# Optimization experiments

Measured on AMD Instinct MI355X. Metric: run time of the kernel, lower is better.

The kernel has to match this reference:

```python
import jax, jax.numpy as jnp
import numpy as np

B, S, D, H, DH = 2, 2048, 2048, 16, 128
ROT_DIM = 128
ROT_BASE = 10000.0
ATTN_SCALE = float(np.sqrt(DH))


def _sin_cos_rotary(n_ctx, rotary_dim, base):
    pos = jnp.arange(n_ctx, dtype=jnp.float32)
    dim = jnp.arange(rotary_dim // 2, dtype=jnp.float32)
    freq = base ** (dim / (rotary_dim / 2))
    freq = jnp.concatenate([freq, freq])  # non-adjacent pairs: '(2 d)' layout
    angles = pos[:, None] / freq[None, :]  # [n_ctx, rotary_dim]
    return jnp.sin(angles), jnp.cos(angles)


def _rotate_every_two(x):
    # non-adjacent-pairs rotation: [-x2, x1] on halves of last dim
    d = x.shape[-1]
    return jnp.concatenate([-x[..., d // 2:], x[..., :d // 2]], axis=-1)


def _apply_rotary(x, sin, cos):
    # x: [batch, pos, head, d_head]
    n = x.shape[1]
    x_rot = x[..., :ROT_DIM]
    x_pass = x[..., ROT_DIM:]
    c = cos[:n][None, :, None, :]
    s = sin[:n][None, :, None, :]
    x_rotated = x_rot * c + _rotate_every_two(x_rot) * s
    return jnp.concatenate([x_rotated, x_pass], axis=-1)


def setup_inputs() -> dict:
    key = jax.random.key(0)
    ks = jax.random.split(key, 8)
    init = 0.02
    return {
        'query_input': jax.random.normal(ks[0], (B, S, D), jnp.float32),
        'key_input': jax.random.normal(ks[1], (B, S, D), jnp.float32),
        'value_input': jax.random.normal(ks[2], (B, S, D), jnp.float32),
        'W_Q': jax.random.normal(ks[3], (H, D, DH), jnp.float32) * init,
        'W_K': jax.random.normal(ks[4], (H, D, DH), jnp.float32) * init,
        'W_V': jax.random.normal(ks[5], (H, D, DH), jnp.float32) * init,
        'W_O': jax.random.normal(ks[6], (H, DH, D), jnp.float32) * init,
        'b_Q': jnp.zeros((H, DH), jnp.float32),
        'b_K': jnp.zeros((H, DH), jnp.float32),
        'b_V': jnp.zeros((H, DH), jnp.float32),
        'b_O': jnp.zeros((D,), jnp.float32),
    }


def reference(query_input, key_input, value_input, W_Q, W_K, W_V, W_O, b_Q, b_K, b_V, b_O):
    # QKV projections: [b, pos, d_model] x [h, d_model, d_head] -> [b, pos, h, d_head]
    q = jnp.einsum('bpd,hde->bphe', query_input, W_Q) + b_Q
    k = jnp.einsum('bpd,hde->bphe', key_input, W_K) + b_K
    v = jnp.einsum('bpd,hde->bphe', value_input, W_V) + b_V

    sin, cos = _sin_cos_rotary(S, ROT_DIM, ROT_BASE)
    q = _apply_rotary(q, sin, cos)
    k = _apply_rotary(k, sin, cos)

    # attention scores [b, h, q_pos, k_pos]
    scores = jnp.einsum('bqhe,bkhe->bhqk', q, k) / ATTN_SCALE
    causal = jnp.tril(jnp.ones((S, S), bool))
    scores = jnp.where(causal[None, None], scores, -jnp.inf)
    pattern = jax.nn.softmax(scores, axis=-1)
    pattern = jnp.where(jnp.isnan(pattern), jnp.zeros_like(pattern), pattern)

    z = jnp.einsum('bhqk,bkhe->bqhe', pattern, v)
    out = jnp.einsum('bqhe,hed->bqd', z, W_O) + b_O
    return out
```

## Files before the change

### kernel.cpp

```cpp
#include <hip/hip_runtime.h>
#include <hip/hip_bf16.h>
#include <cmath>

typedef __bf16 bf16;
typedef __bf16 bf16x8 __attribute__((ext_vector_type(8)));
typedef __bf16 bf16x4 __attribute__((ext_vector_type(4)));
typedef float  f32x4  __attribute__((ext_vector_type(4)));


__global__ void xcvt_kernel(const float* __restrict__ a, const float* __restrict__ b,
                            const float* __restrict__ c,
                            bf16* __restrict__ oa, bf16* __restrict__ ob, bf16* __restrict__ oc) {
    int i = (blockIdx.x * 256 + threadIdx.x) * 4;
    float4 va = *(const float4*)(a + i);
    float4 vb = *(const float4*)(b + i);
    float4 vc = *(const float4*)(c + i);
    bf16x4 ra = { (bf16)va.x, (bf16)va.y, (bf16)va.z, (bf16)va.w };
    bf16x4 rb = { (bf16)vb.x, (bf16)vb.y, (bf16)vb.z, (bf16)vb.w };
    bf16x4 rc = { (bf16)vc.x, (bf16)vc.y, (bf16)vc.z, (bf16)vc.w };
    *(bf16x4*)(oa + i) = ra;
    *(bf16x4*)(ob + i) = rb;
    *(bf16x4*)(oc + i) = rc;
}

__global__ void wtr_kernel(const float* __restrict__ WQ, const float* __restrict__ WK,
                           const float* __restrict__ WV, const float* __restrict__ WO,
                           bf16* __restrict__ WQT, bf16* __restrict__ WKT,
                           bf16* __restrict__ WVT, bf16* __restrict__ WOT) {
    __shared__ float T[64 * 65];
    const int z = blockIdx.y;
    const int bx = blockIdx.x;
    const int tid = threadIdx.x;
    const int tr = tid >> 4;
    const int tc = (tid & 15) * 4;

    const float* src; bf16* dst;
    long sbase, dbase; int sRS;
    if (z < 3) {
        src = (z == 0) ? WQ : (z == 1) ? WK : WV;
        dst = (z == 0) ? WQT : (z == 1) ? WKT : WVT;
        int h = bx >> 6, rem = bx & 63;
        int d0 = (rem >> 1) << 6, e0 = (rem & 1) << 6;
        sbase = (long)h * 262144 + (long)d0 * 128 + e0;
        sRS = 128;
        dbase = (long)(h * 128 + e0) * 2048 + d0;
    } else {
        src = WO; dst = WOT;
        int a0 = (bx >> 5) << 6, b0 = (bx & 31) << 6;
        sbase = (long)a0 * 2048 + b0;
        sRS = 2048;
        dbase = (long)b0 * 2048 + a0;
    }

#pragma unroll
    for (int p = 0; p < 4; p++) {
        int r = p * 16 + tr;
        float4 v = *(const float4*)(src + sbase + (long)r * sRS + tc);
        T[r * 65 + tc]     = v.x;
        T[r * 65 + tc + 1] = v.y;
        T[r * 65 + tc + 2] = v.z;
        T[r * 65 + tc + 3] = v.w;
    }
    __syncthreads();
#pragma unroll
    for (int p = 0; p < 4; p++) {
        int rr = p * 16 + tr;
        bf16x4 o = { (bf16)T[tc * 65 + rr],       (bf16)T[(tc + 1) * 65 + rr],
                     (bf16)T[(tc + 2) * 65 + rr], (bf16)T[(tc + 3) * 65 + rr] };
        *(bf16x4*)(dst + dbase + (long)rr * 2048 + tc) = o;
    }
}

__launch_bounds__(512, 2)
__global__ void qkv_gemm_kernel(const bf16* __restrict__ XQ, const bf16* __restrict__ XK,
                                const bf16* __restrict__ XV,
                                const bf16* __restrict__ WQT, const bf16* __restrict__ WKT,
                                const bf16* __restrict__ WVT,
                                const float* __restrict__ bQ, const float* __restrict__ bK,
                                const float* __restrict__ bV,
                                bf16* __restrict__ QB, bf16* __restrict__ KB,
                                bf16* __restrict__ VT) {
    __shared__ __align__(1024) char SMb[98304];
    const int z = blockIdx.z;
    const bf16* A  = (z == 0) ? XQ  : (z == 1) ? XK  : XV;
    const bf16* Bm = (z == 0) ? WQT : (z == 1) ? WKT : WVT;
    const float* bias = (z == 0) ? bQ : (z == 1) ? bK : bV;

    const int tid = threadIdx.x;
    const int w = tid >> 6, lane = tid & 63;
    const int quad = lane >> 4, l16 = lane & 15;
    const int wm = w & 1, wn = w >> 1;
    const int m_base = blockIdx.x << 8;
    const int h = blockIdx.y;
    const int n_base = h << 7;

    const int lr = lane >> 3;
    const int lc = ((lane & 7) ^ lr) << 3;
    const bf16* gA = A  + (long)(m_base + (w << 4) + lr) * 2048 + lc;
    const bf16* gB = Bm + (long)(n_base + (w << 4) + lr) * 2048 + lc;

#define STAGE_A(T, half) do {                                                                 \
    const bf16* _s = gA + (long)((half) * 128) * 2048 + (T) * 64;                             \
    char* _d = SMb + ((T) & 1) * 32768 + (half) * 16384 + (w << 11);                          \
    __builtin_amdgcn_global_load_lds((const __attribute__((address_space(1))) void*)_s,       \
        (__attribute__((address_space(3))) void*)_d, 16, 0, 0);                               \
    __builtin_amdgcn_global_load_lds((const __attribute__((address_space(1))) void*)(_s + 16384), \
        (__attribute__((address_space(3))) void*)(_d + 1024), 16, 0, 0);                      \
} while (0)
#define STAGE_B(T) do {                                                                       \
    const bf16* _s = gB + (T) * 64;                                                           \
    char* _d = SMb + 65536 + ((T) & 1) * 16384 + (w << 11);                                   \
    __builtin_amdgcn_global_load_lds((const __attribute__((address_space(1))) void*)_s,       \
        (__attribute__((address_space(3))) void*)_d, 16, 0, 0);                               \
    __builtin_amdgcn_global_load_lds((const __attribute__((address_space(1))) void*)(_s + 16384), \
        (__attribute__((address_space(3))) void*)(_d + 1024), 16, 0, 0);                      \
} while (0)
#define RD(buf, row, kh) \
    (*(const bf16x8*)(SMb + (buf) + (row) * 128 + ((((kh) * 64) + cb0) ^ (((row) & 7) << 4))))

    f32x4 acc[8][2] = {};
    bf16x8 af[8], bg[2];
    const int cb0 = quad << 4;
    const int rB0 = wn * 16 + l16;

    STAGE_B(0); STAGE_A(0, 0); STAGE_A(0, 1); STAGE_B(1);
    asm volatile("s_waitcnt vmcnt(2)" ::: "memory");
    __builtin_amdgcn_s_barrier();

    for (int t = 0; t < 32; ++t) {
        const int bufA = (t & 1) * 32768 + wm * 16384;
        const int bufB = 65536 + (t & 1) * 16384;

#pragma unroll
        for (int mt = 0; mt < 8; mt++) af[mt] = RD(bufA, mt * 16 + l16, 0);
        bg[0] = RD(bufB, rB0, 0);
        bg[1] = RD(bufB, rB0 + 64, 0);
        if (t < 31) STAGE_A(t + 1, 0);
        __builtin_amdgcn_s_barrier();
        __builtin_amdgcn_s_setprio(1);
#pragma unroll
        for (int mt = 0; mt < 8; mt++) {
            acc[mt][0] = __builtin_amdgcn_mfma_f32_16x16x32_bf16(af[mt], bg[0], acc[mt][0], 0, 0, 0);
            acc[mt][1] = __builtin_amdgcn_mfma_f32_16x16x32_bf16(af[mt], bg[1], acc[mt][1], 0, 0, 0);
        }
        __builtin_amdgcn_s_setprio(0);
        __builtin_amdgcn_s_barrier();

#pragma unroll
        for (int mt = 0; mt < 8; mt++) af[mt] = RD(bufA, mt * 16 + l16, 1);
        bg[0] = RD(bufB, rB0, 1);
        bg[1] = RD(bufB, rB0 + 64, 1);
        if (t < 31) STAGE_A(t + 1, 1);
        asm volatile("s_waitcnt lgkmcnt(0)" ::: "memory");
        __builtin_amdgcn_sched_barrier(0);
        __builtin_amdgcn_s_barrier();
        if (t < 30) STAGE_B(t + 2);
        __builtin_amdgcn_s_setprio(1);
#pragma unroll
        for (int mt = 0; mt < 8; mt++) {
            acc[mt][0] = __builtin_amdgcn_mfma_f32_16x16x32_bf16(af[mt], bg[0], acc[mt][0], 0, 0, 0);
            acc[mt][1] = __builtin_amdgcn_mfma_f32_16x16x32_bf16(af[mt], bg[1], acc[mt][1], 0, 0, 0);
        }
        __builtin_amdgcn_s_setprio(0);
        if (t == 30) { asm volatile("s_waitcnt vmcnt(0)" ::: "memory"); }
        else         { asm volatile("s_waitcnt vmcnt(2)" ::: "memory"); }
        __builtin_amdgcn_s_barrier();
    }
#undef STAGE_A
#undef STAGE_B
#undef RD

    const int bq = blockIdx.x >> 3;
    const long obase = ((long)(bq * 16 + h)) << 18;

    if (z <= 1) {
        bf16* O = (z == 0) ? QB : KB;
        const float scl = (z == 0) ? 0.08838834764831845f : 1.0f;
        const int e_lo = wn * 16 + l16;
        const float bv_lo = bias[n_base + e_lo];
        const float bv_hi = bias[n_base + e_lo + 64];
        const float inv_freq = exp2f((float)e_lo * -0.20762050593046f);
#pragma unroll
        for (int mt = 0; mt < 8; mt++) {
#pragma unroll
            for (int r = 0; r < 4; r++) {
                int s = (m_base & 2047) + wm * 128 + mt * 16 + quad * 4 + r;
                float sn, cs;
                __sincosf((float)s * inv_freq, &sn, &cs);
                float x0 = acc[mt][0][r] + bv_lo;
                float x1 = acc[mt][1][r] + bv_hi;
                O[obase + ((long)s << 7) + e_lo]      = (bf16)((x0 * cs - x1 * sn) * scl);
                O[obase + ((long)s << 7) + e_lo + 64] = (bf16)((x1 * cs + x0 * sn) * scl);
            }
        }
    } else {
        bf16* Ct = (bf16*)SMb;
#pragma unroll
        for (int nt = 0; nt < 2; nt++) {
            const int e_l = nt * 64 + wn * 16 + l16;
            const float bv = bias[n_base + e_l];
#pragma unroll
            for (int mt = 0; mt < 8; mt++) {
                int s0 = wm * 128 + mt * 16 + quad * 4;
                bf16x4 pk = { (bf16)(acc[mt][nt][0] + bv), (bf16)(acc[mt][nt][1] + bv),
                              (bf16)(acc[mt][nt][2] + bv), (bf16)(acc[mt][nt][3] + bv) };
                *(bf16x4*)&Ct[e_l * 264 + s0] = pk;
            }
        }
        __syncthreads();
        {
            const int e_l = tid >> 2;
            const int sq  = (tid & 3) << 6;
            const long vb = obase + ((long)e_l << 11) + (m_base & 2047) + sq;
#pragma unroll
            for (int j = 0; j < 8; j++)
                *(bf16x8*)&VT[vb + j * 8] = *(const bf16x8*)&Ct[e_l * 264 + sq + j * 8];
        }
    }
}

__launch_bounds__(256, 3)
__global__ void flash_kernel(const bf16* __restrict__ Q, const bf16* __restrict__ K,
                             const bf16* __restrict__ Vt, bf16* __restrict__ Z) {
    __shared__ __align__(16) bf16 Ks[64 * 136];
    __shared__ __align__(16) bf16 Vs[128 * 72];
    __shared__ __align__(16) bf16 Ps[64 * 72];
    const int tid = threadIdx.x, w = tid >> 6, lane = tid & 63;
    const int quad = lane >> 4, l16 = lane & 15;
    const int n = blockIdx.x;
    const int bh = (n & 7) | (((n >> 3) & 3) << 3);
    const int qt = 31 - (n >> 5);
    const int b = bh >> 4, h = bh & 15;
    const long qk_base = (long)bh << 18;
    const int qbase = qt << 6;
    const float FM = 12.0f;

    const int kr_row = tid >> 4;
    const int kr_col = (tid & 15) << 3;
    const int vr_row = tid >> 3;
    const int vr_col = (tid & 7) << 3;
    const bf16* Kg = K  + qk_base + (long)kr_row * 128 + kr_col;
    const bf16* Vg = Vt + qk_base + (long)vr_row * 2048 + vr_col;

    bf16x8 qf[4];
#pragma unroll
    for (int ks = 0; ks < 4; ks++)
        qf[ks] = *(const bf16x8*)(Q + qk_base + ((long)(qbase + w * 16 + l16) << 7) + ks * 32 + (quad << 3));

    bf16x8 va[4], ka[4], vb2[4], kb[4];
#pragma unroll
    for (int p = 0; p < 4; p++) va[p] = *(const bf16x8*)(Vg + (long)p * 65536);
#pragma unroll
    for (int p = 0; p < 4; p++) ka[p] = *(const bf16x8*)(Kg + (long)(p * 16) * 128);

    f32x4 o[8] = {};
    float lsum[4] = {0.f, 0.f, 0.f, 0.f};

    for (int kt = 0; kt <= qt; kt++) {
#pragma unroll
        for (int p = 0; p < 4; p++)
            *(bf16x8*)&Vs[(p * 32 + vr_row) * 72 + vr_col] = va[p];
#pragma unroll
        for (int p = 0; p < 4; p++)
            *(bf16x8*)&Ks[(p * 16 + kr_row) * 136 + kr_col] = ka[p];
        if (kt < qt) {
            const long koff = (long)(kt + 1) * 64;
#pragma unroll
            for (int p = 0; p < 4; p++) vb2[p] = *(const bf16x8*)(Vg + (long)p * 65536 + koff);
#pragma unroll
            for (int p = 0; p < 4; p++) kb[p] = *(const bf16x8*)(Kg + (koff + p * 16) * 128);
        }
        __syncthreads();

        f32x4 sc[4] = {};
#pragma unroll
        for (int nt = 0; nt < 4; nt++)
#pragma unroll
            for (int ks = 0; ks < 4; ks++) {
                bf16x8 kf = *(const bf16x8*)&Ks[(nt * 16 + l16) * 136 + ks * 32 + (quad << 3)];
                sc[nt] = __builtin_amdgcn_mfma_f32_16x16x32_bf16(qf[ks], kf, sc[nt], 0, 0, 0);
            }

        if (kt == qt) {
#pragma unroll
            for (int nt = 0; nt < 4; nt++)
#pragma unroll
                for (int r = 0; r < 4; r++) {
                    int qrow = qbase + w * 16 + quad * 4 + r;
                    int kv = (qt << 6) + nt * 16 + l16;
                    if (kv > qrow) sc[nt][r] = -3.0e38f;
                }
        }

#pragma unroll
        for (int nt = 0; nt < 4; nt++)
#pragma unroll
            for (int r = 0; r < 4; r++) {
                float p = __expf(sc[nt][r] - FM);
                lsum[r] += p;
                Ps[(w * 16 + quad * 4 + r) * 72 + nt * 16 + l16] = (bf16)p;
            }

#pragma unroll
        for (int kk = 0; kk < 2; kk++) {
            bf16x8 pf = *(const bf16x8*)&Ps[(w * 16 + l16) * 72 + kk * 32 + (quad << 3)];
#pragma unroll
            for (int dt = 0; dt < 8; dt++) {
                bf16x8 vf = *(const bf16x8*)&Vs[(dt * 16 + l16) * 72 + kk * 32 + (quad << 3)];
                o[dt] = __builtin_amdgcn_mfma_f32_16x16x32_bf16(pf, vf, o[dt], 0, 0, 0);
            }
        }
        __syncthreads();

#pragma unroll
        for (int p = 0; p < 4; p++) va[p] = vb2[p];
#pragma unroll
        for (int p = 0; p < 4; p++) ka[p] = kb[p];
    }

#pragma unroll
    for (int r = 0; r < 4; r++) {
        float l = lsum[r];
        l += __shfl_xor(l, 1);
        l += __shfl_xor(l, 2);
        l += __shfl_xor(l, 4);
        l += __shfl_xor(l, 8);
        float inv = 1.f / l;
        int qrow = qbase + w * 16 + quad * 4 + r;
        long zr = ((long)(b * 2048 + qrow) << 11) + h * 128;
#pragma unroll
        for (int dt = 0; dt < 8; dt++)
            Z[zr + dt * 16 + l16] = (bf16)(o[dt][r] * inv);
    }
}

__launch_bounds__(256)
__global__ void gemm_o_kernel(const bf16* __restrict__ A, const bf16* __restrict__ Bm,
                              const float* __restrict__ bias, float* __restrict__ Of) {
    __shared__ __align__(16) bf16 As[128 * 32];
    __shared__ __align__(16) bf16 Bs[128 * 32];
    const int tid = threadIdx.x;
    const int w = tid >> 6, lane = tid & 63;
    const int quad = lane >> 4, l16 = lane & 15;
    const int wm = w & 1, wn = w >> 1;
    const int m_base = blockIdx.x << 7, n_base = blockIdx.y << 7;

    const int srow = lane >> 2;
    const int scol = (lane & 3) << 3;
    const int ab0 = w * 2, ab1 = w * 2 + 1;
    const bf16* gA0 = A  + (long)(m_base + ab0 * 16 + srow) * 2048 + scol;
    const bf16* gA1 = A  + (long)(m_base + ab1 * 16 + srow) * 2048 + scol;
    const bf16* gB0 = Bm + (long)(n_base + ab0 * 16 + srow) * 2048 + scol;
    const bf16* gB1 = Bm + (long)(n_base + ab1 * 16 + srow) * 2048 + scol;
    bf16* lA0 = &As[ab0 * 512];
    bf16* lA1 = &As[ab1 * 512];
    bf16* lB0 = &Bs[ab0 * 512];
    bf16* lB1 = &Bs[ab1 * 512];

    f32x4 acc[4][4] = {};

    for (int k0 = 0; k0 < 2048; k0 += 32) {
        __builtin_amdgcn_global_load_lds((const __attribute__((address_space(1))) void*)(gA0 + k0),
                                         (__attribute__((address_space(3))) void*)lA0, 16, 0, 0);
        __builtin_amdgcn_global_load_lds((const __attribute__((address_space(1))) void*)(gA1 + k0),
                                         (__attribute__((address_space(3))) void*)lA1, 16, 0, 0);
        __builtin_amdgcn_global_load_lds((const __attribute__((address_space(1))) void*)(gB0 + k0),
                                         (__attribute__((address_space(3))) void*)lB0, 16, 0, 0);
        __builtin_amdgcn_global_load_lds((const __attribute__((address_space(1))) void*)(gB1 + k0),
                                         (__attribute__((address_space(3))) void*)lB1, 16, 0, 0);
        __syncthreads();

        bf16x8 af[4], bfr[4];
#pragma unroll
        for (int mt = 0; mt < 4; mt++)
            af[mt] = *(const bf16x8*)&As[((wm * 64 + mt * 16 + l16) << 5) + (quad << 3)];
#pragma unroll
        for (int nt = 0; nt < 4; nt++)
            bfr[nt] = *(const bf16x8*)&Bs[((wn * 64 + nt * 16 + l16) << 5) + (quad << 3)];
#pragma unroll
        for (int mt = 0; mt < 4; mt++)
#pragma unroll
            for (int nt = 0; nt < 4; nt++)
                acc[mt][nt] = __builtin_amdgcn_mfma_f32_16x16x32_bf16(af[mt], bfr[nt], acc[mt][nt], 0, 0, 0);
        __syncthreads();
    }

#pragma unroll
    for (int nt = 0; nt < 4; nt++) {
        int col = n_base + wn * 64 + nt * 16 + l16;
        float bv = bias[col];
#pragma unroll
        for (int mt = 0; mt < 4; mt++) {
#pragma unroll
            for (int r = 0; r < 4; r++) {
                int row = m_base + wm * 64 + mt * 16 + quad * 4 + r;
                Of[((long)row << 11) + col] = acc[mt][nt][r] + bv;
            }
        }
    }
}

extern "C" void kernel_launch(void* const* d_in, const int* in_sizes, int n_in,
                              void* d_out, int out_size, void* d_ws, size_t ws_size,
                              hipStream_t stream) {
    (void)in_sizes; (void)n_in; (void)out_size; (void)ws_size;
    const float* qin = (const float*)d_in[0];
    const float* kin = (const float*)d_in[1];
    const float* vin = (const float*)d_in[2];
    const float* WQ  = (const float*)d_in[3];
    const float* WK  = (const float*)d_in[4];
    const float* WV  = (const float*)d_in[5];
    const float* WO  = (const float*)d_in[6];
    const float* bQ  = (const float*)d_in[7];
    const float* bK  = (const float*)d_in[8];
    const float* bV  = (const float*)d_in[9];
    const float* bO  = (const float*)d_in[10];
    float* out = (float*)d_out;

    bf16* ws = (bf16*)d_ws;
    bf16* XQ  = ws + 0L;
    bf16* XK  = ws + 8388608L;
    bf16* XV  = ws + 16777216L;
    bf16* WQT = ws + 25165824L;
    bf16* WKT = ws + 29360128L;
    bf16* WVT = ws + 33554432L;
    bf16* WOT = ws + 37748736L;
    bf16* QB  = ws + 41943040L;
    bf16* KB  = ws + 50331648L;
    bf16* VT  = ws + 58720256L;
    bf16* Z   = XQ;

    xcvt_kernel<<<8192, 256, 0, stream>>>(qin, kin, vin, XQ, XK, XV);
    wtr_kernel<<<dim3(1024, 4), 256, 0, stream>>>(WQ, WK, WV, WO, WQT, WKT, WVT, WOT);
    qkv_gemm_kernel<<<dim3(16, 16, 3), 512, 0, stream>>>(XQ, XK, XV, WQT, WKT, WVT,
                                                         bQ, bK, bV, QB, KB, VT);
    flash_kernel<<<1024, 256, 0, stream>>>(QB, KB, VT, Z);
    gemm_o_kernel<<<dim3(32, 16), 256, 0, stream>>>(Z, WOT, bO, out);
}
```

Baseline: 428.3 us.

## Process two query tiles per flash block and rewrite output GEMM with triple-buffered LDS

The flash kernel now handles a 128-row query super-tile per block, covering two 64-row sub-tiles. Each K/V tile is loaded once and reused for both, which halves K/V traffic and the block count, at the cost of more registers (occupancy hint lowered to 2). The output-projection GEMM is rewritten with 256x128 tiles, 512 threads, a triple-buffered 144KB LDS pipeline fed by global_load_lds with XOR swizzling, and explicit vmcnt waits. It also raises priority around the MFMA section. This aims to hide memory latency and cut bank conflicts, but the large LDS footprint limits residency.

```diff
diff --git a/kernel.cpp b/kernel.cpp
--- a/kernel.cpp
+++ b/kernel.cpp
@@ -219,7 +219,104 @@
     }
 }
 
-__launch_bounds__(256, 3)
+#define GLOAD(S, D) __builtin_amdgcn_global_load_lds( \
+    (const __attribute__((address_space(1))) void*)(S), \
+    (__attribute__((address_space(3))) void*)(D), 16, 0, 0)
+
+#define STAGE_T(T, slotOff) do {                                     \
+    const bf16* _sa = gA + (long)(T) * 64;                           \
+    char* _da = SMb + (slotOff) + (w << 12);                         \
+    GLOAD(_sa,         _da);                                         \
+    GLOAD(_sa + 16384, _da + 1024);                                  \
+    GLOAD(_sa + 32768, _da + 2048);                                  \
+    GLOAD(_sa + 49152, _da + 3072);                                  \
+    const bf16* _sb = gB + (long)(T) * 64;                           \
+    char* _db = SMb + (slotOff) + 32768 + (w << 11);                 \
+    GLOAD(_sb,         _db);                                         \
+    GLOAD(_sb + 16384, _db + 1024);                                  \
+} while (0)
+
+#define RD_A(r, kh) (*(const bf16x8*)(SMb + curS + (r) * 128 + ((((kh) << 6) + cb0) ^ sw)))
+#define RD_B(r, kh) (*(const bf16x8*)(SMb + curS + 32768 + (r) * 128 + ((((kh) << 6) + cb0) ^ sw)))
+
+__launch_bounds__(512, 2)
+__global__ void gemm_o_kernel(const bf16* __restrict__ A, const bf16* __restrict__ Bm,
+                              const float* __restrict__ bias, float* __restrict__ Of) {
+    __shared__ __align__(1024) char SMb[147456];
+    const int tid = threadIdx.x;
+    const int w = tid >> 6, lane = tid & 63;
+    const int quad = lane >> 4, l16 = lane & 15;
+    const int wm = w >> 1, wn = w & 1;
+    const int m_base = blockIdx.x << 8;
+    const int n_base = blockIdx.y << 7;
+
+    const int lr = lane >> 3;
+    const int lc = ((lane & 7) ^ lr) << 3;
+    const bf16* gA = A  + (long)(m_base + (w << 5) + lr) * 2048 + lc;
+    const bf16* gB = Bm + (long)(n_base + (w << 4) + lr) * 2048 + lc;
+
+    f32x4 acc[4][4] = {};
+    const int cb0 = quad << 4;
+    const int sw  = (l16 & 7) << 4;
+    STAGE_T(0, 0);
+    STAGE_T(1, 49152);
+    asm volatile("s_waitcnt vmcnt(6)" ::: "memory");
+    int curS = 0, stgS = 98304;
+#pragma unroll 1
+    for (int t = 0; t < 32; ++t) {
+        __builtin_amdgcn_s_barrier();
+        __builtin_amdgcn_sched_barrier(0);
+        if (t < 30) STAGE_T(t + 2, stgS);
+        bf16x8 bgf[2][2][2];
+#pragma unroll
+        for (int hi = 0; hi < 2; hi++)
+#pragma unroll
+            for (int nt2 = 0; nt2 < 2; nt2++) {
+                int rB = wn * 32 + nt2 * 16 + hi * 64 + l16;
+                bgf[hi][nt2][0] = RD_B(rB, 0);
+                bgf[hi][nt2][1] = RD_B(rB, 1);
+            }
+        __builtin_amdgcn_s_setprio(1);
+#pragma unroll
+        for (int mt = 0; mt < 4; mt++) {
+            int rA = wm * 64 + mt * 16 + l16;
+            bf16x8 a0 = RD_A(rA, 0);
+            bf16x8 a1 = RD_A(rA, 1);
+#pragma unroll
+            for (int hi = 0; hi < 2; hi++)
+#pragma unroll
+                for (int nt2 = 0; nt2 < 2; nt2++) {
+                    acc[mt][hi * 2 + nt2] = __builtin_amdgcn_mfma_f32_16x16x32_bf16(
+                        a0, bgf[hi][nt2][0], acc[mt][hi * 2 + nt2], 0, 0, 0);
+                    acc[mt][hi * 2 + nt2] = __builtin_amdgcn_mfma_f32_16x16x32_bf16(
+                        a1, bgf[hi][nt2][1], acc[mt][hi * 2 + nt2], 0, 0, 0);
+                }
+        }
+        __builtin_amdgcn_s_setprio(0);
+        if (t == 30) { asm volatile("s_waitcnt vmcnt(0)" ::: "memory"); }
+        else         { asm volatile("s_waitcnt vmcnt(6)" ::: "memory"); }
+        curS = (curS == 98304) ? 0 : curS + 49152;
+        stgS = (stgS == 98304) ? 0 : stgS + 49152;
+    }
+
+#pragma unroll
+    for (int hi = 0; hi < 2; hi++)
+#pragma unroll
+        for (int nt2 = 0; nt2 < 2; nt2++) {
+            int col = n_base + wn * 32 + nt2 * 16 + hi * 64 + l16;
+            float bv = bias[col];
+#pragma unroll
+            for (int mt = 0; mt < 4; mt++) {
+#pragma unroll
+                for (int r = 0; r < 4; r++) {
+                    int row = m_base + wm * 64 + mt * 16 + quad * 4 + r;
+                    Of[((long)row << 11) + col] = acc[mt][hi * 2 + nt2][r] + bv;
+                }
+            }
+        }
+}
+
+__launch_bounds__(256, 2)
 __global__ void flash_kernel(const bf16* __restrict__ Q, const bf16* __restrict__ K,
                              const bf16* __restrict__ Vt, bf16* __restrict__ Z) {
     __shared__ __align__(16) bf16 Ks[64 * 136];
@@ -228,11 +325,12 @@
     const int tid = threadIdx.x, w = tid >> 6, lane = tid & 63;
     const int quad = lane >> 4, l16 = lane & 15;
     const int n = blockIdx.x;
-    const int bh = (n & 7) | (((n >> 3) & 3) << 3);
-    const int qt = 31 - (n >> 5);
+    const int bh = n & 31;
+    const int qsup = 15 - (n >> 5);
     const int b = bh >> 4, h = bh & 15;
     const long qk_base = (long)bh << 18;
-    const int qbase = qt << 6;
+    const int Q0 = qsup << 7;
+    const int NT = 2 * qsup + 2;
     const float FM = 12.0f;
 
     const int kr_row = tid >> 4;
@@ -242,10 +340,13 @@
     const bf16* Kg = K  + qk_base + (long)kr_row * 128 + kr_col;
     const bf16* Vg = Vt + qk_base + (long)vr_row * 2048 + vr_col;
 
-    bf16x8 qf[4];
-#pragma unroll
-    for (int ks = 0; ks < 4; ks++)
-        qf[ks] = *(const bf16x8*)(Q + qk_base + ((long)(qbase + w * 16 + l16) << 7) + ks * 32 + (quad << 3));
+    bf16x8 qf[2][4];
+#pragma unroll
+    for (int qs = 0; qs < 2; qs++)
+#pragma unroll
+        for (int ks = 0; ks < 4; ks++)
+            qf[qs][ks] = *(const bf16x8*)(Q + qk_base
+                + ((long)(Q0 + qs * 64 + w * 16 + l16) << 7) + ks * 32 + (quad << 3));
 
     bf16x8 va[4], ka[4], vb2[4], kb[4];
 #pragma unroll
@@ -253,17 +354,17 @@
 #pragma unroll
     for (int p = 0; p < 4; p++) ka[p] = *(const bf16x8*)(Kg + (long)(p * 16) * 128);
 
-    f32x4 o[8] = {};
-    float lsum[4] = {0.f, 0.f, 0.f, 0.f};
-
-    for (int kt = 0; kt <= qt; kt++) {
+    f32x4 o[2][8] = {};
+    float lsum[2][4] = {};
+
+    for (int kt = 0; kt < NT; kt++) {
 #pragma unroll
         for (int p = 0; p < 4; p++)
             *(bf16x8*)&Vs[(p * 32 + vr_row) * 72 + vr_col] = va[p];
 #pragma unroll
         for (int p = 0; p < 4; p++)
             *(bf16x8*)&Ks[(p * 16 + kr_row) * 136 + kr_col] = ka[p];
-        if (kt < qt) {
+        if (kt + 1 < NT) {
             const long koff = (long)(kt + 1) * 64;
 #pragma unroll
             for (int p = 0; p < 4; p++) vb2[p] = *(const bf16x8*)(Vg + (long)p * 65536 + koff);
@@ -272,42 +373,51 @@
         }
         __syncthreads();
 
-        f32x4 sc[4] = {};
-#pragma unroll
-        for (int nt = 0; nt < 4; nt++)
-#pragma unroll
-            for (int ks = 0; ks < 4; ks++) {
-                bf16x8 kf = *(const bf16x8*)&Ks[(nt * 16 + l16) * 136 + ks * 32 + (quad << 3)];
-                sc[nt] = __builtin_amdgcn_mfma_f32_16x16x32_bf16(qf[ks], kf, sc[nt], 0, 0, 0);
-            }
-
-        if (kt == qt) {
+        const bool diag0 = (kt == 2 * qsup);
+        const bool skip0 = (kt == 2 * qsup + 1);
+
+#pragma unroll
+        for (int qs = 0; qs < 2; qs++) {
+            if (qs == 0 && skip0) continue;
+
+            f32x4 sc[4] = {};
 #pragma unroll
             for (int nt = 0; nt < 4; nt++)
 #pragma unroll
+                for (int ks = 0; ks < 4; ks++) {
+                    bf16x8 kf = *(const bf16x8*)&Ks[(nt * 16 + l16) * 136 + ks * 32 + (quad << 3)];
+                    sc[nt] = __builtin_amdgcn_mfma_f32_16x16x32_bf16(qf[qs][ks], kf, sc[nt], 0, 0, 0);
+                }
+
+            const bool dg = (qs == 0) ? diag0 : skip0;
+            if (dg) {
+#pragma unroll
+                for (int nt = 0; nt < 4; nt++)
+#pragma unroll
+                    for (int r = 0; r < 4; r++) {
+                        int qrow = Q0 + qs * 64 + w * 16 + quad * 4 + r;
+                        int kv = kt * 64 + nt * 16 + l16;
+                        if (kv > qrow) sc[nt][r] = -3.0e38f;
+                    }
+            }
+
+#pragma unroll
+            for (int nt = 0; nt < 4; nt++)
+#pragma unroll
                 for (int r = 0; r < 4; r++) {
-                    int qrow = qbase + w * 16 + quad * 4 + r;
-                    int kv = (qt << 6) + nt * 16 + l16;
-                    if (kv > qrow) sc[nt][r] = -3.0e38f;
+                    float p = __expf(sc[nt][r] - FM);
+                    lsum[qs][r] += p;
+                    Ps[(w * 16 + quad * 4 + r) * 72 + nt * 16 + l16] = (bf16)p;
                 }
-        }
-
-#pragma unroll
-        for (int nt = 0; nt < 4; nt++)
-#pragma unroll
-            for (int r = 0; r < 4; r++) {
-                float p = __expf(sc[nt][r] - FM);
-                lsum[r] += p;
-                Ps[(w * 16 + quad * 4 + r) * 72 + nt * 16 + l16] = (bf16)p;
-            }
-
-#pragma unroll
-        for (int kk = 0; kk < 2; kk++) {
-            bf16x8 pf = *(const bf16x8*)&Ps[(w * 16 + l16) * 72 + kk * 32 + (quad << 3)];
-#pragma unroll
-            for (int dt = 0; dt < 8; dt++) {
-                bf16x8 vf = *(const bf16x8*)&Vs[(dt * 16 + l16) * 72 + kk * 32 + (quad << 3)];
-                o[dt] = __builtin_amdgcn_mfma_f32_16x16x32_bf16(pf, vf, o[dt], 0, 0, 0);
+
+#pragma unroll
+            for (int kk = 0; kk < 2; kk++) {
+                bf16x8 pf = *(const bf16x8*)&Ps[(w * 16 + l16) * 72 + kk * 32 + (quad << 3)];
+#pragma unroll
+                for (int dt = 0; dt < 8; dt++) {
+                    bf16x8 vf = *(const bf16x8*)&Vs[(dt * 16 + l16) * 72 + kk * 32 + (quad << 3)];
+                    o[qs][dt] = __builtin_amdgcn_mfma_f32_16x16x32_bf16(pf, vf, o[qs][dt], 0, 0, 0);
+                }
             }
         }
         __syncthreads();
@@ -319,85 +429,21 @@
     }
 
 #pragma unroll
-    for (int r = 0; r < 4; r++) {
-        float l = lsum[r];
-        l += __shfl_xor(l, 1);
-        l += __shfl_xor(l, 2);
-        l += __shfl_xor(l, 4);
-        l += __shfl_xor(l, 8);
-        float inv = 1.f / l;
-        int qrow = qbase + w * 16 + quad * 4 + r;
-        long zr = ((long)(b * 2048 + qrow) << 11) + h * 128;
-#pragma unroll
-        for (int dt = 0; dt < 8; dt++)
-            Z[zr + dt * 16 + l16] = (bf16)(o[dt][r] * inv);
-    }
-}
-
-__launch_bounds__(256)
-__global__ void gemm_o_kernel(const bf16* __restrict__ A, const bf16* __restrict__ Bm,
-                              const float* __restrict__ bias, float* __restrict__ Of) {
-    __shared__ __align__(16) bf16 As[128 * 32];
-    __shared__ __align__(16) bf16 Bs[128 * 32];
-    const int tid = threadIdx.x;
-    const int w = tid >> 6, lane = tid & 63;
-    const int quad = lane >> 4, l16 = lane & 15;
-    const int wm = w & 1, wn = w >> 1;
-    const int m_base = blockIdx.x << 7, n_base = blockIdx.y << 7;
-
-    const int srow = lane >> 2;
-    const int scol = (lane & 3) << 3;
-    const int ab0 = w * 2, ab1 = w * 2 + 1;
-    const bf16* gA0 = A  + (long)(m_base + ab0 * 16 + srow) * 2048 + scol;
-    const bf16* gA1 = A  + (long)(m_base + ab1 * 16 + srow) * 2048 + scol;
-    const bf16* gB0 = Bm + (long)(n_base + ab0 * 16 + srow) * 2048 + scol;
-    const bf16* gB1 = Bm + (long)(n_base + ab1 * 16 + srow) * 2048 + scol;
-    bf16* lA0 = &As[ab0 * 512];
-    bf16* lA1 = &As[ab1 * 512];
-    bf16* lB0 = &Bs[ab0 * 512];
-    bf16* lB1 = &Bs[ab1 * 512];
-
-    f32x4 acc[4][4] = {};
-
-    for (int k0 = 0; k0 < 2048; k0 += 32) {
-        __builtin_amdgcn_global_load_lds((const __attribute__((address_space(1))) void*)(gA0 + k0),
-                                         (__attribute__((address_space(3))) void*)lA0, 16, 0, 0);
-        __builtin_amdgcn_global_load_lds((const __attribute__((address_space(1))) void*)(gA1 + k0),
-                                         (__attribute__((address_space(3))) void*)lA1, 16, 0, 0);
-        __builtin_amdgcn_global_load_lds((const __attribute__((address_space(1))) void*)(gB0 + k0),
-                                         (__attribute__((address_space(3))) void*)lB0, 16, 0, 0);
-        __builtin_amdgcn_global_load_lds((const __attribute__((address_space(1))) void*)(gB1 + k0),
-                                         (__attribute__((address_space(3))) void*)lB1, 16, 0, 0);
-        __syncthreads();
-
-        bf16x8 af[4], bfr[4];
-#pragma unroll
-        for (int mt = 0; mt < 4; mt++)
-            af[mt] = *(const bf16x8*)&As[((wm * 64 + mt * 16 + l16) << 5) + (quad << 3)];
-#pragma unroll
-        for (int nt = 0; nt < 4; nt++)
-            bfr[nt] = *(const bf16x8*)&Bs[((wn * 64 + nt * 16 + l16) << 5) + (quad << 3)];
-#pragma unroll
-        for (int mt = 0; mt < 4; mt++)
-#pragma unroll
-            for (int nt = 0; nt < 4; nt++)
-                acc[mt][nt] = __builtin_amdgcn_mfma_f32_16x16x32_bf16(af[mt], bfr[nt], acc[mt][nt], 0, 0, 0);
-        __syncthreads();
-    }
-
-#pragma unroll
-    for (int nt = 0; nt < 4; nt++) {
-        int col = n_base + wn * 64 + nt * 16 + l16;
-        float bv = bias[col];
-#pragma unroll
-        for (int mt = 0; mt < 4; mt++) {
-#pragma unroll
-            for (int r = 0; r < 4; r++) {
-                int row = m_base + wm * 64 + mt * 16 + quad * 4 + r;
-                Of[((long)row << 11) + col] = acc[mt][nt][r] + bv;
-            }
-        }
-    }
+    for (int qs = 0; qs < 2; qs++)
+#pragma unroll
+        for (int r = 0; r < 4; r++) {
+            float l = lsum[qs][r];
+            l += __shfl_xor(l, 1);
+            l += __shfl_xor(l, 2);
+            l += __shfl_xor(l, 4);
+            l += __shfl_xor(l, 8);
+            float inv = 1.f / l;
+            int qrow = Q0 + qs * 64 + w * 16 + quad * 4 + r;
+            long zr = ((long)(b * 2048 + qrow) << 11) + h * 128;
+#pragma unroll
+            for (int dt = 0; dt < 8; dt++)
+                Z[zr + dt * 16 + l16] = (bf16)(o[qs][dt][r] * inv);
+        }
 }
 
 extern "C" void kernel_launch(void* const* d_in, const int* in_sizes, int n_in,
@@ -434,6 +480,6 @@
     wtr_kernel<<<dim3(1024, 4), 256, 0, stream>>>(WQ, WK, WV, WO, WQT, WKT, WVT, WOT);
     qkv_gemm_kernel<<<dim3(16, 16, 3), 512, 0, stream>>>(XQ, XK, XV, WQT, WKT, WVT,
                                                          bQ, bK, bV, QB, KB, VT);
-    flash_kernel<<<1024, 256, 0, stream>>>(QB, KB, VT, Z);
-    gemm_o_kernel<<<dim3(32, 16), 256, 0, stream>>>(Z, WOT, bO, out);
-}
+    flash_kernel<<<512, 256, 0, stream>>>(QB, KB, VT, Z);
+    gemm_o_kernel<<<dim3(16, 16), 512, 0, stream>>>(Z, WOT, bO, out);
+}
```

After: 438.1 us. +2.3%, slower.
